# Optimization experiments

Hardware: AMD Instinct MI355X
Metric: run time of the kernel (lower is better)

## Reference

```python
import jax, jax.numpy as jnp
import numpy as np

B, N, F_IN, F_OUT = 16, 1024, 128, 128

def setup_inputs() -> dict:
    key = jax.random.key(0)
    k1, k2, k3 = jax.random.split(key, 3)
    X = jax.random.normal(k1, (B, N, F_IN), dtype=jnp.float32)
    A = jax.random.uniform(k2, (B, N, N), dtype=jnp.float32)
    W = jax.random.normal(k3, (F_IN, F_OUT), dtype=jnp.float32)
    return {"X": X, "A": A, "W": W}

def reference(X, A, W):
    # A_hat = A + I  (batched add of identity)
    n = A.shape[-1]
    A_hat = A + jnp.eye(n, dtype=A.dtype)  # [B,N,N]
    # D_hat^{-1/2} applied as elementwise row/col scaling (torch builds diag
    # matrices and inverts; mathematically identical for diagonal D).
    deg = jnp.sum(A_hat, axis=-1)               # [B,N]
    d_inv_sqrt = 1.0 / jnp.sqrt(deg)            # [B,N]
    A_norm = A_hat * d_inv_sqrt[:, :, None] * d_inv_sqrt[:, None, :]  # [B,N,N]
    out = jnp.einsum('bnm,bmf->bnf', A_norm, X)  # aggregation bmm
    out = jnp.einsum('bnf,fg->bng', out, W)      # weight matmul
    return out
```

## Files before the change

kernel.cpp:

```cpp
#include <hip/hip_runtime.h>

#define NN 1024
#define FF 128

typedef __attribute__((ext_vector_type(8))) short bf16x8;
typedef __attribute__((ext_vector_type(4))) float f32x4;

__device__ __forceinline__ unsigned short f2bf(float x) {
  unsigned u = __float_as_uint(x);
  u += 0x7fff + ((u >> 16) & 1);
  return (unsigned short)(u >> 16);
}
__device__ __forceinline__ float bf2f(unsigned short b) {
  return __uint_as_float(((unsigned)b) << 16);
}
__device__ __forceinline__ bf16x8 cvt8(float4 a, float4 b) {
  bf16x8 r;
  r[0] = (short)f2bf(a.x); r[1] = (short)f2bf(a.y);
  r[2] = (short)f2bf(a.z); r[3] = (short)f2bf(a.w);
  r[4] = (short)f2bf(b.x); r[5] = (short)f2bf(b.y);
  r[6] = (short)f2bf(b.z); r[7] = (short)f2bf(b.w);
  return r;
}

__device__ __forceinline__ void gl_lds16(const void* g, void* l) {
  __builtin_amdgcn_global_load_lds(
      (const __attribute__((address_space(1))) unsigned*)g,
      (__attribute__((address_space(3))) unsigned*)l, 16, 0, 0);
}

__global__ __launch_bounds__(256) void k_deg(const float* __restrict__ A,
                                             const float* __restrict__ W,
                                             float* __restrict__ d,
                                             unsigned short* __restrict__ Wt) {
  if (blockIdx.x >= 4096) {
    int id = (blockIdx.x - 4096) * 256 + threadIdx.x;
    int g = id >> 7, f = id & 127;
    Wt[g * 128 + f] = f2bf(W[f * 128 + g]);
    return;
  }
  int row  = blockIdx.x * 4 + (threadIdx.x >> 6);
  int lane = threadIdx.x & 63;
  const float4* Ar = (const float4*)(A + (size_t)row * NN);
  float s = 0.f;
#pragma unroll
  for (int i = 0; i < 4; ++i) {
    float4 v = Ar[lane + i * 64];
    s += (v.x + v.y) + (v.z + v.w);
  }
#pragma unroll
  for (int off = 32; off > 0; off >>= 1) s += __shfl_down(s, off, 64);
  if (lane == 0) d[row] = rsqrtf(s + 1.0f);
}

__global__ __launch_bounds__(256) void k_xw(const float* __restrict__ X,
                                            const unsigned short* __restrict__ Wt,
                                            const float* __restrict__ d,
                                            unsigned short* __restrict__ Yt) {
  __shared__ __align__(16) unsigned short Xs[64 * 128];
  __shared__ __align__(16) unsigned short Ws[128 * 128];
  __shared__ float dl[64];
  int t  = threadIdx.x;
  int b  = blockIdx.x >> 4;
  int m0 = (blockIdx.x & 15) * 64;

#pragma unroll
  for (int j = 0; j < 4; ++j) {
    int id = t + j * 256;
    int r = id >> 4, p = id & 15, c = p ^ (r & 15);
    const float* gp = X + ((size_t)(b * NN + m0 + r) * FF + c * 8);
    float4 v0 = *(const float4*)gp;
    float4 v1 = *(const float4*)(gp + 4);
    *(bf16x8*)&Xs[r * 128 + p * 8] = cvt8(v0, v1);
  }
#pragma unroll
  for (int j = 0; j < 8; ++j) {
    int id = t + j * 256;
    int g = id >> 4, p = id & 15, c = p ^ (g & 15);
    uint4 v = *(const uint4*)(Wt + g * 128 + c * 8);
    *(uint4*)&Ws[g * 128 + p * 8] = v;
  }
  if (t < 64) dl[t] = d[b * NN + m0 + t];
  __syncthreads();

  int wave = t >> 6, lane = t & 63, quad = lane >> 4, l16 = lane & 15;
  f32x4 acc[8];
#pragma unroll
  for (int ct = 0; ct < 8; ++ct) acc[ct] = (f32x4){0.f, 0.f, 0.f, 0.f};

#pragma unroll
  for (int ks = 0; ks < 4; ++ks) {
    int q = ks * 4 + quad;
    bf16x8 a = *(const bf16x8*)&Xs[(wave * 16 + l16) * 128 + (q ^ l16) * 8];
#pragma unroll
    for (int ct = 0; ct < 8; ++ct) {
      bf16x8 w = *(const bf16x8*)&Ws[(ct * 16 + l16) * 128 + (q ^ l16) * 8];
      acc[ct] = __builtin_amdgcn_mfma_f32_16x16x32_bf16(a, w, acc[ct], 0, 0, 0);
    }
  }

  int mb = wave * 16 + quad * 4;
  float4 d4 = *(const float4*)&dl[mb];
#pragma unroll
  for (int ct = 0; ct < 8; ++ct) {
    int g = ct * 16 + l16;
    ushort4 p;
    p.x = f2bf(d4.x * acc[ct][0]);
    p.y = f2bf(d4.y * acc[ct][1]);
    p.z = f2bf(d4.z * acc[ct][2]);
    p.w = f2bf(d4.w * acc[ct][3]);
    *(ushort4*)(Yt + (size_t)(b * 128 + g) * NN + m0 + mb) = p;
  }
}

__global__ __launch_bounds__(256) void k_agg(const float* __restrict__ A,
                                             const unsigned short* __restrict__ Yt,
                                             const float* __restrict__ d,
                                             float* __restrict__ out) {
  __shared__ __align__(16) float          Asf[3][32 * 64];
  __shared__ __align__(16) unsigned short Ys[3][128 * 64];
  int t   = threadIdx.x;
  int bid = blockIdx.x;
  int xcd = bid & 7;
  int j   = bid >> 3;
  int b   = xcd + 8 * (j >> 5);
  int n0  = (j & 31) * 32;
  int wave = t >> 6, lane = t & 63, quad = lane >> 4, l16 = lane & 15;
  int wr = wave >> 1, wc = wave & 1;

  const float*          Ab = A  + (size_t)(b * NN + n0) * NN;
  const unsigned short* Yb = Yt + (size_t)b * 128 * NN;

  int ra = lane >> 4, pa_s = lane & 15;
  int ry_s = lane >> 3, py_s = lane & 7;

  auto issue = [&](int k0, int bufi) {
#pragma unroll
    for (int jj = 0; jj < 2; ++jj) {
      int r = wave * 8 + jj * 4 + ra;
      int c = pa_s ^ (2 * (r & 7));
      gl_lds16(Ab + ((size_t)r * NN + k0 + c * 4), &Asf[bufi][(wave * 8 + jj * 4) * 64]);
    }
#pragma unroll
    for (int jj = 0; jj < 4; ++jj) {
      int ry = wave * 32 + jj * 8 + ry_s;
      int c  = py_s ^ (ry & 7);
      gl_lds16(Yb + ((size_t)ry * NN + k0 + c * 8), &Ys[bufi][(wave * 32 + jj * 8) * 64]);
    }
  };

  f32x4 acc[4];
#pragma unroll
  for (int ct = 0; ct < 4; ++ct) acc[ct] = (f32x4){0.f, 0.f, 0.f, 0.f};

  int swA = 2 * (l16 & 7);
  issue(0, 0);
  issue(64, 1);

#pragma unroll
  for (int s = 0; s < 16; ++s) {
    if (s < 15) asm volatile("s_waitcnt vmcnt(6)" ::: "memory");
    else        asm volatile("s_waitcnt vmcnt(0)" ::: "memory");
    __builtin_amdgcn_s_barrier();
    const float*          as = &Asf[s % 3][0];
    const unsigned short* ys = &Ys[s % 3][0];
    __builtin_amdgcn_s_setprio(1);
#pragma unroll
    for (int ks = 0; ks < 2; ++ks) {
      int cq = ks * 4 + quad;
      int pa = (2 * cq) ^ swA;
      float4 a0 = *(const float4*)&as[(wr * 16 + l16) * 64 + pa * 4];
      float4 a1 = *(const float4*)&as[(wr * 16 + l16) * 64 + pa * 4 + 4];
      bf16x8 a = cvt8(a0, a1);
#pragma unroll
      for (int ct = 0; ct < 4; ++ct) {
        int cp = (cq ^ (l16 & 7)) * 8;
        bf16x8 y = *(const bf16x8*)&ys[(wc * 64 + ct * 16 + l16) * 64 + cp];
        acc[ct] = __builtin_amdgcn_mfma_f32_16x16x32_bf16(a, y, acc[ct], 0, 0, 0);
      }
    }
    __builtin_amdgcn_s_setprio(0);
    __builtin_amdgcn_sched_barrier(0);
    if (s < 14) issue((s + 2) * 64, (s + 2) % 3);
  }

  int nb = n0 + wr * 16 + quad * 4;
  float4 d4 = *(const float4*)(d + b * NN + nb);
#pragma unroll
  for (int ct = 0; ct < 4; ++ct) {
    int g = wc * 64 + ct * 16 + l16;
    ushort4 yv = *(const ushort4*)(Yt + (size_t)(b * 128 + g) * NN + nb);
    float* op = out + ((size_t)(b * NN + nb) * FF + g);
    op[0 * FF] = d4.x * (acc[ct][0] + bf2f(yv.x));
    op[1 * FF] = d4.y * (acc[ct][1] + bf2f(yv.y));
    op[2 * FF] = d4.z * (acc[ct][2] + bf2f(yv.z));
    op[3 * FF] = d4.w * (acc[ct][3] + bf2f(yv.w));
  }
}

extern "C" void kernel_launch(void* const* d_in, const int* in_sizes, int n_in,
                              void* d_out, int out_size, void* d_ws, size_t ws_size,
                              hipStream_t stream) {
  const float* X = (const float*)d_in[0];
  const float* A = (const float*)d_in[1];
  const float* W = (const float*)d_in[2];
  float* out = (float*)d_out;

  char* ws = (char*)d_ws;
  float*          dinv = (float*)ws;
  unsigned short* Wt   = (unsigned short*)(ws + 65536);
  unsigned short* Yt   = (unsigned short*)(ws + 98304);

  k_deg<<<dim3(4096 + 64), dim3(256), 0, stream>>>(A, W, dinv, Wt);
  k_xw <<<dim3(256),       dim3(256), 0, stream>>>(X, Wt, dinv, Yt);
  k_agg<<<dim3(512),       dim3(256), 0, stream>>>(A, Yt, dinv, out);
}
```

Measured before the change: 118.9 us.

## Fuse XW and aggregation kernels with a device-wide grid barrier

Merges the X·W projection kernel and the A·Y aggregation kernel into one persistent launch of 512 blocks. The projection work is split across twice as many blocks (half the output columns each), and a global atomic barrier separates it from the aggregation. This saves one kernel launch and its drain/fill gap, but adds a spin-wait grid sync that relies on all 512 blocks being co-resident (two per CU with the larger shared buffer).

```diff
diff --git a/kernel.cpp b/kernel.cpp
--- a/kernel.cpp
+++ b/kernel.cpp
@@ -2,6 +2,7 @@
 
 #define NN 1024
 #define FF 128
+#define NBLK 512
 
 typedef __attribute__((ext_vector_type(8))) short bf16x8;
 typedef __attribute__((ext_vector_type(4))) float f32x4;
@@ -29,11 +30,34 @@
       (__attribute__((address_space(3))) unsigned*)l, 16, 0, 0);
 }
 
+__device__ __forceinline__ void gsync(unsigned* sync) {
+  __syncthreads();
+  if (threadIdx.x == 0) {
+    unsigned g0 = __hip_atomic_load(&sync[1], __ATOMIC_RELAXED,
+                                    __HIP_MEMORY_SCOPE_AGENT);
+    unsigned my = __hip_atomic_fetch_add(&sync[0], 1u, __ATOMIC_ACQ_REL,
+                                         __HIP_MEMORY_SCOPE_AGENT);
+    if (my == NBLK - 1) {
+      __hip_atomic_store(&sync[0], 0u, __ATOMIC_RELAXED,
+                         __HIP_MEMORY_SCOPE_AGENT);
+      __hip_atomic_fetch_add(&sync[1], 1u, __ATOMIC_RELEASE,
+                             __HIP_MEMORY_SCOPE_AGENT);
+    } else {
+      while (__hip_atomic_load(&sync[1], __ATOMIC_ACQUIRE,
+                               __HIP_MEMORY_SCOPE_AGENT) == g0)
+        __builtin_amdgcn_s_sleep(2);
+    }
+  }
+  __syncthreads();
+}
+
 __global__ __launch_bounds__(256) void k_deg(const float* __restrict__ A,
                                              const float* __restrict__ W,
                                              float* __restrict__ d,
-                                             unsigned short* __restrict__ Wt) {
+                                             unsigned short* __restrict__ Wt,
+                                             unsigned* __restrict__ sync) {
   if (blockIdx.x >= 4096) {
+    if (blockIdx.x == 4096 && threadIdx.x < 2) sync[threadIdx.x] = 0u;
     int id = (blockIdx.x - 4096) * 256 + threadIdx.x;
     int g = id >> 7, f = id & 127;
     Wt[g * 128 + f] = f2bf(W[f * 128 + g]);
@@ -53,148 +77,152 @@
   if (lane == 0) d[row] = rsqrtf(s + 1.0f);
 }
 
-__global__ __launch_bounds__(256) void k_xw(const float* __restrict__ X,
-                                            const unsigned short* __restrict__ Wt,
-                                            const float* __restrict__ d,
-                                            unsigned short* __restrict__ Yt) {
-  __shared__ __align__(16) unsigned short Xs[64 * 128];
-  __shared__ __align__(16) unsigned short Ws[128 * 128];
-  __shared__ float dl[64];
-  int t  = threadIdx.x;
-  int b  = blockIdx.x >> 4;
-  int m0 = (blockIdx.x & 15) * 64;
-
-#pragma unroll
-  for (int j = 0; j < 4; ++j) {
-    int id = t + j * 256;
-    int r = id >> 4, p = id & 15, c = p ^ (r & 15);
-    const float* gp = X + ((size_t)(b * NN + m0 + r) * FF + c * 8);
-    float4 v0 = *(const float4*)gp;
-    float4 v1 = *(const float4*)(gp + 4);
-    *(bf16x8*)&Xs[r * 128 + p * 8] = cvt8(v0, v1);
-  }
-#pragma unroll
-  for (int j = 0; j < 8; ++j) {
-    int id = t + j * 256;
-    int g = id >> 4, p = id & 15, c = p ^ (g & 15);
-    uint4 v = *(const uint4*)(Wt + g * 128 + c * 8);
-    *(uint4*)&Ws[g * 128 + p * 8] = v;
-  }
-  if (t < 64) dl[t] = d[b * NN + m0 + t];
-  __syncthreads();
-
+__global__ __launch_bounds__(256, 2) void k_fused(const float* __restrict__ X,
+                                                  const float* __restrict__ A,
+                                                  const unsigned short* __restrict__ Wt,
+                                                  const float* __restrict__ d,
+                                                  unsigned short* __restrict__ Yt,
+                                                  float* __restrict__ out,
+                                                  unsigned* __restrict__ sync) {
+  __shared__ __align__(16) char smem[73728];
+  int t = threadIdx.x;
+  int bid = blockIdx.x;
   int wave = t >> 6, lane = t & 63, quad = lane >> 4, l16 = lane & 15;
-  f32x4 acc[8];
-#pragma unroll
-  for (int ct = 0; ct < 8; ++ct) acc[ct] = (f32x4){0.f, 0.f, 0.f, 0.f};
-
-#pragma unroll
-  for (int ks = 0; ks < 4; ++ks) {
-    int q = ks * 4 + quad;
-    bf16x8 a = *(const bf16x8*)&Xs[(wave * 16 + l16) * 128 + (q ^ l16) * 8];
-#pragma unroll
-    for (int ct = 0; ct < 8; ++ct) {
-      bf16x8 w = *(const bf16x8*)&Ws[(ct * 16 + l16) * 128 + (q ^ l16) * 8];
-      acc[ct] = __builtin_amdgcn_mfma_f32_16x16x32_bf16(a, w, acc[ct], 0, 0, 0);
-    }
-  }
-
-  int mb = wave * 16 + quad * 4;
-  float4 d4 = *(const float4*)&dl[mb];
-#pragma unroll
-  for (int ct = 0; ct < 8; ++ct) {
-    int g = ct * 16 + l16;
-    ushort4 p;
-    p.x = f2bf(d4.x * acc[ct][0]);
-    p.y = f2bf(d4.y * acc[ct][1]);
-    p.z = f2bf(d4.z * acc[ct][2]);
-    p.w = f2bf(d4.w * acc[ct][3]);
-    *(ushort4*)(Yt + (size_t)(b * 128 + g) * NN + m0 + mb) = p;
-  }
-}
-
-__global__ __launch_bounds__(256) void k_agg(const float* __restrict__ A,
-                                             const unsigned short* __restrict__ Yt,
-                                             const float* __restrict__ d,
-                                             float* __restrict__ out) {
-  __shared__ __align__(16) float          Asf[3][32 * 64];
-  __shared__ __align__(16) unsigned short Ys[3][128 * 64];
-  int t   = threadIdx.x;
-  int bid = blockIdx.x;
-  int xcd = bid & 7;
-  int j   = bid >> 3;
-  int b   = xcd + 8 * (j >> 5);
-  int n0  = (j & 31) * 32;
-  int wave = t >> 6, lane = t & 63, quad = lane >> 4, l16 = lane & 15;
-  int wr = wave >> 1, wc = wave & 1;
-
-  const float*          Ab = A  + (size_t)(b * NN + n0) * NN;
-  const unsigned short* Yb = Yt + (size_t)b * 128 * NN;
-
-  int ra = lane >> 4, pa_s = lane & 15;
-  int ry_s = lane >> 3, py_s = lane & 7;
-
-  auto issue = [&](int k0, int bufi) {
-#pragma unroll
-    for (int jj = 0; jj < 2; ++jj) {
-      int r = wave * 8 + jj * 4 + ra;
-      int c = pa_s ^ (2 * (r & 7));
-      gl_lds16(Ab + ((size_t)r * NN + k0 + c * 4), &Asf[bufi][(wave * 8 + jj * 4) * 64]);
-    }
-#pragma unroll
-    for (int jj = 0; jj < 4; ++jj) {
-      int ry = wave * 32 + jj * 8 + ry_s;
-      int c  = py_s ^ (ry & 7);
-      gl_lds16(Yb + ((size_t)ry * NN + k0 + c * 8), &Ys[bufi][(wave * 32 + jj * 8) * 64]);
-    }
-  };
-
-  f32x4 acc[4];
-#pragma unroll
-  for (int ct = 0; ct < 4; ++ct) acc[ct] = (f32x4){0.f, 0.f, 0.f, 0.f};
-
-  int swA = 2 * (l16 & 7);
-  issue(0, 0);
-  issue(64, 1);
-
-#pragma unroll
-  for (int s = 0; s < 16; ++s) {
-    if (s < 15) asm volatile("s_waitcnt vmcnt(6)" ::: "memory");
-    else        asm volatile("s_waitcnt vmcnt(0)" ::: "memory");
-    __builtin_amdgcn_s_barrier();
-    const float*          as = &Asf[s % 3][0];
-    const unsigned short* ys = &Ys[s % 3][0];
-    __builtin_amdgcn_s_setprio(1);
-#pragma unroll
-    for (int ks = 0; ks < 2; ++ks) {
-      int cq = ks * 4 + quad;
-      int pa = (2 * cq) ^ swA;
-      float4 a0 = *(const float4*)&as[(wr * 16 + l16) * 64 + pa * 4];
-      float4 a1 = *(const float4*)&as[(wr * 16 + l16) * 64 + pa * 4 + 4];
-      bf16x8 a = cvt8(a0, a1);
+
+  {
+    unsigned short* Xs = (unsigned short*)smem;
+    unsigned short* Ws = (unsigned short*)(smem + 16384);
+    float*          dl = (float*)(smem + 32768);
+    int job = bid >> 1, gh = bid & 1;
+    int xb = job >> 4, m0 = (job & 15) * 64;
+
+#pragma unroll
+    for (int j = 0; j < 4; ++j) {
+      int id = t + j * 256;
+      int r = id >> 4, p = id & 15, c = p ^ (r & 15);
+      const float* gp = X + ((size_t)(xb * NN + m0 + r) * FF + c * 8);
+      float4 v0 = *(const float4*)gp;
+      float4 v1 = *(const float4*)(gp + 4);
+      *(bf16x8*)&Xs[r * 128 + p * 8] = cvt8(v0, v1);
+    }
+#pragma unroll
+    for (int j = 0; j < 4; ++j) {
+      int id = t + j * 256;
+      int gl = id >> 4, p = id & 15, c = p ^ (gl & 15);
+      uint4 v = *(const uint4*)(Wt + (size_t)(gh * 64 + gl) * 128 + c * 8);
+      *(uint4*)&Ws[gl * 128 + p * 8] = v;
+    }
+    if (t < 64) dl[t] = d[xb * NN + m0 + t];
+    __syncthreads();
+
+    f32x4 acc[4];
+#pragma unroll
+    for (int ct = 0; ct < 4; ++ct) acc[ct] = (f32x4){0.f, 0.f, 0.f, 0.f};
+#pragma unroll
+    for (int ks = 0; ks < 4; ++ks) {
+      int q = ks * 4 + quad;
+      bf16x8 a = *(const bf16x8*)&Xs[(wave * 16 + l16) * 128 + (q ^ l16) * 8];
 #pragma unroll
       for (int ct = 0; ct < 4; ++ct) {
-        int cp = (cq ^ (l16 & 7)) * 8;
-        bf16x8 y = *(const bf16x8*)&ys[(wc * 64 + ct * 16 + l16) * 64 + cp];
-        acc[ct] = __builtin_amdgcn_mfma_f32_16x16x32_bf16(a, y, acc[ct], 0, 0, 0);
-      }
-    }
-    __builtin_amdgcn_s_setprio(0);
-    __builtin_amdgcn_sched_barrier(0);
-    if (s < 14) issue((s + 2) * 64, (s + 2) % 3);
-  }
-
-  int nb = n0 + wr * 16 + quad * 4;
-  float4 d4 = *(const float4*)(d + b * NN + nb);
-#pragma unroll
-  for (int ct = 0; ct < 4; ++ct) {
-    int g = wc * 64 + ct * 16 + l16;
-    ushort4 yv = *(const ushort4*)(Yt + (size_t)(b * 128 + g) * NN + nb);
-    float* op = out + ((size_t)(b * NN + nb) * FF + g);
-    op[0 * FF] = d4.x * (acc[ct][0] + bf2f(yv.x));
-    op[1 * FF] = d4.y * (acc[ct][1] + bf2f(yv.y));
-    op[2 * FF] = d4.z * (acc[ct][2] + bf2f(yv.z));
-    op[3 * FF] = d4.w * (acc[ct][3] + bf2f(yv.w));
+        bf16x8 w = *(const bf16x8*)&Ws[(ct * 16 + l16) * 128 + (q ^ l16) * 8];
+        acc[ct] = __builtin_amdgcn_mfma_f32_16x16x32_bf16(a, w, acc[ct], 0, 0, 0);
+      }
+    }
+    int mb = wave * 16 + quad * 4;
+    float4 d4 = *(const float4*)&dl[mb];
+#pragma unroll
+    for (int ct = 0; ct < 4; ++ct) {
+      int g = gh * 64 + ct * 16 + l16;
+      ushort4 p;
+      p.x = f2bf(d4.x * acc[ct][0]);
+      p.y = f2bf(d4.y * acc[ct][1]);
+      p.z = f2bf(d4.z * acc[ct][2]);
+      p.w = f2bf(d4.w * acc[ct][3]);
+      *(ushort4*)(Yt + (size_t)(xb * 128 + g) * NN + m0 + mb) = p;
+    }
+  }
+
+  gsync(sync);
+
+  {
+    float*          Asf = (float*)smem;
+    unsigned short* Ys  = (unsigned short*)(smem + 24576);
+    int xcd = bid & 7;
+    int j   = bid >> 3;
+    int b   = xcd + 8 * (j >> 5);
+    int n0  = (j & 31) * 32;
+    int wr = wave >> 1, wc = wave & 1;
+
+    const float*          Ab = A  + (size_t)(b * NN + n0) * NN;
+    const unsigned short* Yb = Yt + (size_t)b * 128 * NN;
+
+    int ra = lane >> 4, pa_s = lane & 15;
+    int ry_s = lane >> 3, py_s = lane & 7;
+
+    auto issue = [&](int k0, int bufi) {
+#pragma unroll
+      for (int jj = 0; jj < 2; ++jj) {
+        int r = wave * 8 + jj * 4 + ra;
+        int c = pa_s ^ (2 * (r & 7));
+        gl_lds16(Ab + ((size_t)r * NN + k0 + c * 4),
+                 &Asf[bufi * 2048 + (wave * 8 + jj * 4) * 64]);
+      }
+#pragma unroll
+      for (int jj = 0; jj < 4; ++jj) {
+        int ry = wave * 32 + jj * 8 + ry_s;
+        int c  = py_s ^ (ry & 7);
+        gl_lds16(Yb + ((size_t)ry * NN + k0 + c * 8),
+                 &Ys[bufi * 8192 + (wave * 32 + jj * 8) * 64]);
+      }
+    };
+
+    f32x4 acc[4];
+#pragma unroll
+    for (int ct = 0; ct < 4; ++ct) acc[ct] = (f32x4){0.f, 0.f, 0.f, 0.f};
+
+    int swA = 2 * (l16 & 7);
+    issue(0, 0);
+    issue(64, 1);
+
+#pragma unroll
+    for (int s = 0; s < 16; ++s) {
+      if (s < 15) asm volatile("s_waitcnt vmcnt(6)" ::: "memory");
+      else        asm volatile("s_waitcnt vmcnt(0)" ::: "memory");
+      __builtin_amdgcn_s_barrier();
+      const float*          as = &Asf[(s % 3) * 2048];
+      const unsigned short* ys = &Ys[(s % 3) * 8192];
+      __builtin_amdgcn_s_setprio(1);
+#pragma unroll
+      for (int ks = 0; ks < 2; ++ks) {
+        int cq = ks * 4 + quad;
+        int pa = (2 * cq) ^ swA;
+        float4 a0 = *(const float4*)&as[(wr * 16 + l16) * 64 + pa * 4];
+        float4 a1 = *(const float4*)&as[(wr * 16 + l16) * 64 + pa * 4 + 4];
+        bf16x8 a = cvt8(a0, a1);
+#pragma unroll
+        for (int ct = 0; ct < 4; ++ct) {
+          int cp = (cq ^ (l16 & 7)) * 8;
+          bf16x8 y = *(const bf16x8*)&ys[(wc * 64 + ct * 16 + l16) * 64 + cp];
+          acc[ct] = __builtin_amdgcn_mfma_f32_16x16x32_bf16(a, y, acc[ct], 0, 0, 0);
+        }
+      }
+      __builtin_amdgcn_s_setprio(0);
+      __builtin_amdgcn_sched_barrier(0);
+      if (s < 14) issue((s + 2) * 64, (s + 2) % 3);
+    }
+
+    int nb = n0 + wr * 16 + quad * 4;
+    float4 d4 = *(const float4*)(d + b * NN + nb);
+#pragma unroll
+    for (int ct = 0; ct < 4; ++ct) {
+      int g = wc * 64 + ct * 16 + l16;
+      ushort4 yv = *(const ushort4*)(Yt + (size_t)(b * 128 + g) * NN + nb);
+      float* op = out + ((size_t)(b * NN + nb) * FF + g);
+      op[0 * FF] = d4.x * (acc[ct][0] + bf2f(yv.x));
+      op[1 * FF] = d4.y * (acc[ct][1] + bf2f(yv.y));
+      op[2 * FF] = d4.z * (acc[ct][2] + bf2f(yv.z));
+      op[3 * FF] = d4.w * (acc[ct][3] + bf2f(yv.w));
+    }
   }
 }
 
@@ -210,8 +238,8 @@
   float*          dinv = (float*)ws;
   unsigned short* Wt   = (unsigned short*)(ws + 65536);
   unsigned short* Yt   = (unsigned short*)(ws + 98304);
-
-  k_deg<<<dim3(4096 + 64), dim3(256), 0, stream>>>(A, W, dinv, Wt);
-  k_xw <<<dim3(256),       dim3(256), 0, stream>>>(X, Wt, dinv, Yt);
-  k_agg<<<dim3(512),       dim3(256), 0, stream>>>(A, Yt, dinv, out);
-}
+  unsigned*       sync = (unsigned*)(ws + 4292608);
+
+  k_deg  <<<dim3(4096 + 64), dim3(256), 0, stream>>>(A, W, dinv, Wt, sync);
+  k_fused<<<dim3(NBLK),      dim3(256), 0, stream>>>(X, A, Wt, dinv, Yt, out, sync);
+}
```

New measurement: 178.9 us. 50.5% more time.

## Merge degree and XW kernels, apply column scaling inside aggregation

Applied to the files above, without the earlier changes.

Folds the degree reduction and the X·W GEMM into one launch by dropping the dependency of XW on d. The column normalisation moves into the aggregation kernel, which now scales each A tile by d in registers before the bf16 conversion, and the identity term is rescaled in the epilogue. The W transpose is done inside each XW block. This removes one kernel launch and one serialization point, at the cost of extra LDS reads and multiplies in the aggregation hot loop and a redundant per-block W transpose with scattered LDS writes.

```diff
diff --git a/kernel.cpp b/kernel.cpp
--- a/kernel.cpp
+++ b/kernel.cpp
@@ -29,37 +29,29 @@
       (__attribute__((address_space(3))) unsigned*)l, 16, 0, 0);
 }
 
-__global__ __launch_bounds__(256) void k_deg(const float* __restrict__ A,
-                                             const float* __restrict__ W,
-                                             float* __restrict__ d,
-                                             unsigned short* __restrict__ Wt) {
-  if (blockIdx.x >= 4096) {
-    int id = (blockIdx.x - 4096) * 256 + threadIdx.x;
-    int g = id >> 7, f = id & 127;
-    Wt[g * 128 + f] = f2bf(W[f * 128 + g]);
+__global__ __launch_bounds__(256) void k_degxw(const float* __restrict__ A,
+                                               const float* __restrict__ X,
+                                               const float* __restrict__ W,
+                                               float* __restrict__ d,
+                                               unsigned short* __restrict__ Yt) {
+  if (blockIdx.x >= 256) {
+    int row  = (blockIdx.x - 256) * 4 + (threadIdx.x >> 6);
+    int lane = threadIdx.x & 63;
+    const float4* Ar = (const float4*)(A + (size_t)row * NN);
+    float s = 0.f;
+#pragma unroll
+    for (int i = 0; i < 4; ++i) {
+      float4 v = Ar[lane + i * 64];
+      s += (v.x + v.y) + (v.z + v.w);
+    }
+#pragma unroll
+    for (int off = 32; off > 0; off >>= 1) s += __shfl_down(s, off, 64);
+    if (lane == 0) d[row] = rsqrtf(s + 1.0f);
     return;
   }
-  int row  = blockIdx.x * 4 + (threadIdx.x >> 6);
-  int lane = threadIdx.x & 63;
-  const float4* Ar = (const float4*)(A + (size_t)row * NN);
-  float s = 0.f;
-#pragma unroll
-  for (int i = 0; i < 4; ++i) {
-    float4 v = Ar[lane + i * 64];
-    s += (v.x + v.y) + (v.z + v.w);
-  }
-#pragma unroll
-  for (int off = 32; off > 0; off >>= 1) s += __shfl_down(s, off, 64);
-  if (lane == 0) d[row] = rsqrtf(s + 1.0f);
-}
-
-__global__ __launch_bounds__(256) void k_xw(const float* __restrict__ X,
-                                            const unsigned short* __restrict__ Wt,
-                                            const float* __restrict__ d,
-                                            unsigned short* __restrict__ Yt) {
+
   __shared__ __align__(16) unsigned short Xs[64 * 128];
   __shared__ __align__(16) unsigned short Ws[128 * 128];
-  __shared__ float dl[64];
   int t  = threadIdx.x;
   int b  = blockIdx.x >> 4;
   int m0 = (blockIdx.x & 15) * 64;
@@ -73,14 +65,22 @@
     float4 v1 = *(const float4*)(gp + 4);
     *(bf16x8*)&Xs[r * 128 + p * 8] = cvt8(v0, v1);
   }
-#pragma unroll
-  for (int j = 0; j < 8; ++j) {
-    int id = t + j * 256;
-    int g = id >> 4, p = id & 15, c = p ^ (g & 15);
-    uint4 v = *(const uint4*)(Wt + g * 128 + c * 8);
-    *(uint4*)&Ws[g * 128 + p * 8] = v;
-  }
-  if (t < 64) dl[t] = d[b * NN + m0 + t];
+  {
+    int f = t >> 1, gh = (t & 1) * 64;
+    const float* wrow = W + (size_t)f * FF + gh;
+    int c8 = (f >> 3);
+    int e  = f & 7;
+#pragma unroll
+    for (int j4 = 0; j4 < 16; ++j4) {
+      float4 wv = *(const float4*)(wrow + j4 * 4);
+#pragma unroll
+      for (int k = 0; k < 4; ++k) {
+        int g = gh + j4 * 4 + k;
+        float v = (k == 0) ? wv.x : (k == 1) ? wv.y : (k == 2) ? wv.z : wv.w;
+        Ws[g * 128 + ((c8 ^ (g & 15)) * 8) + e] = f2bf(v);
+      }
+    }
+  }
   __syncthreads();
 
   int wave = t >> 6, lane = t & 63, quad = lane >> 4, l16 = lane & 15;
@@ -100,15 +100,14 @@
   }
 
   int mb = wave * 16 + quad * 4;
-  float4 d4 = *(const float4*)&dl[mb];
 #pragma unroll
   for (int ct = 0; ct < 8; ++ct) {
     int g = ct * 16 + l16;
     ushort4 p;
-    p.x = f2bf(d4.x * acc[ct][0]);
-    p.y = f2bf(d4.y * acc[ct][1]);
-    p.z = f2bf(d4.z * acc[ct][2]);
-    p.w = f2bf(d4.w * acc[ct][3]);
+    p.x = f2bf(acc[ct][0]);
+    p.y = f2bf(acc[ct][1]);
+    p.z = f2bf(acc[ct][2]);
+    p.w = f2bf(acc[ct][3]);
     *(ushort4*)(Yt + (size_t)(b * 128 + g) * NN + m0 + mb) = p;
   }
 }
@@ -119,6 +118,7 @@
                                              float* __restrict__ out) {
   __shared__ __align__(16) float          Asf[3][32 * 64];
   __shared__ __align__(16) unsigned short Ys[3][128 * 64];
+  __shared__ __align__(16) float          dl[NN];
   int t   = threadIdx.x;
   int bid = blockIdx.x;
   int xcd = bid & 7;
@@ -131,6 +131,9 @@
   const float*          Ab = A  + (size_t)(b * NN + n0) * NN;
   const unsigned short* Yb = Yt + (size_t)b * 128 * NN;
 
+  *(float4*)&dl[t * 4] = *(const float4*)(d + (size_t)b * NN + t * 4);
+  __syncthreads();
+
   int ra = lane >> 4, pa_s = lane & 15;
   int ry_s = lane >> 3, py_s = lane & 7;
 
@@ -164,6 +167,7 @@
     __builtin_amdgcn_s_barrier();
     const float*          as = &Asf[s % 3][0];
     const unsigned short* ys = &Ys[s % 3][0];
+    int k0 = s * 64;
     __builtin_amdgcn_s_setprio(1);
 #pragma unroll
     for (int ks = 0; ks < 2; ++ks) {
@@ -171,6 +175,10 @@
       int pa = (2 * cq) ^ swA;
       float4 a0 = *(const float4*)&as[(wr * 16 + l16) * 64 + pa * 4];
       float4 a1 = *(const float4*)&as[(wr * 16 + l16) * 64 + pa * 4 + 4];
+      float4 dv0 = *(const float4*)&dl[k0 + cq * 8];
+      float4 dv1 = *(const float4*)&dl[k0 + cq * 8 + 4];
+      a0.x *= dv0.x; a0.y *= dv0.y; a0.z *= dv0.z; a0.w *= dv0.w;
+      a1.x *= dv1.x; a1.y *= dv1.y; a1.z *= dv1.z; a1.w *= dv1.w;
       bf16x8 a = cvt8(a0, a1);
 #pragma unroll
       for (int ct = 0; ct < 4; ++ct) {
@@ -185,16 +193,16 @@
   }
 
   int nb = n0 + wr * 16 + quad * 4;
-  float4 d4 = *(const float4*)(d + b * NN + nb);
+  float4 d4 = *(const float4*)&dl[nb];
 #pragma unroll
   for (int ct = 0; ct < 4; ++ct) {
     int g = wc * 64 + ct * 16 + l16;
     ushort4 yv = *(const ushort4*)(Yt + (size_t)(b * 128 + g) * NN + nb);
     float* op = out + ((size_t)(b * NN + nb) * FF + g);
-    op[0 * FF] = d4.x * (acc[ct][0] + bf2f(yv.x));
-    op[1 * FF] = d4.y * (acc[ct][1] + bf2f(yv.y));
-    op[2 * FF] = d4.z * (acc[ct][2] + bf2f(yv.z));
-    op[3 * FF] = d4.w * (acc[ct][3] + bf2f(yv.w));
+    op[0 * FF] = d4.x * (acc[ct][0] + d4.x * bf2f(yv.x));
+    op[1 * FF] = d4.y * (acc[ct][1] + d4.y * bf2f(yv.y));
+    op[2 * FF] = d4.z * (acc[ct][2] + d4.z * bf2f(yv.z));
+    op[3 * FF] = d4.w * (acc[ct][3] + d4.w * bf2f(yv.w));
   }
 }
 
@@ -208,10 +216,8 @@
 
   char* ws = (char*)d_ws;
   float*          dinv = (float*)ws;
-  unsigned short* Wt   = (unsigned short*)(ws + 65536);
-  unsigned short* Yt   = (unsigned short*)(ws + 98304);
-
-  k_deg<<<dim3(4096 + 64), dim3(256), 0, stream>>>(A, W, dinv, Wt);
-  k_xw <<<dim3(256),       dim3(256), 0, stream>>>(X, Wt, dinv, Yt);
-  k_agg<<<dim3(512),       dim3(256), 0, stream>>>(A, Yt, dinv, out);
-}
+  unsigned short* Yt   = (unsigned short*)(ws + 65536);
+
+  k_degxw<<<dim3(256 + 4096), dim3(256), 0, stream>>>(A, X, W, dinv, Yt);
+  k_agg  <<<dim3(512),        dim3(256), 0, stream>>>(A, Yt, dinv, out);
+}
```

After: 117.6 us (median of 2 runs). No clear change (-1.0%).
